# Kernel optimization log

Measured on AMD Instinct MI355X. Metric: run time of the kernel, lower is better.

Reference implementation:

```python
import jax, jax.numpy as jnp
import numpy as np

B, SQ, SKV, D, H = 4, 2048, 2048, 1024, 16
DH = D // H  # 64


def setup_inputs() -> dict:
    key = jax.random.key(0)
    ks = jax.random.split(key, 8)
    s = 0.02  # realistic init scale for weights
    return {
        "query": jax.random.normal(ks[0], (B, SQ, D), dtype=jnp.float32),
        "value": jax.random.normal(ks[1], (B, SKV, D), dtype=jnp.float32),
        "wq": jax.random.normal(ks[2], (H, D, DH), dtype=jnp.float32) * s,
        "bq": jnp.zeros((H, DH), dtype=jnp.float32),
        "wk": jax.random.normal(ks[3], (H, D, DH), dtype=jnp.float32) * s,
        "bk": jnp.zeros((H, DH), dtype=jnp.float32),
        "wv": jax.random.normal(ks[4], (H, D, DH), dtype=jnp.float32) * s,
        "bv": jnp.zeros((H, DH), dtype=jnp.float32),
        "wo": jax.random.normal(ks[5], (D, D), dtype=jnp.float32) * s,
        "bo": jnp.zeros((D,), dtype=jnp.float32),
    }


def reference(query, value, wq, bq, wk, bk, wv, bv, wo, bo):
    # Batched equivalent of the per-head Dense loop: [B,S,D] x [H,D,DH] -> [B,H,S,DH]
    q = jnp.einsum("bsd,hde->bhse", query, wq) + bq[None, :, None, :]
    k = jnp.einsum("bsd,hde->bhse", value, wk) + bk[None, :, None, :]
    v = jnp.einsum("bsd,hde->bhse", value, wv) + bv[None, :, None, :]
    scale = 1.0 / jnp.sqrt(jnp.asarray(DH, dtype=q.dtype))
    scores = jnp.einsum("bhqe,bhke->bhqk", q, k) * scale  # [B,H,SQ,SKV]
    align = jax.nn.softmax(scores, axis=-1)
    heads = jnp.einsum("bhqk,bhke->bhqe", align, v)  # [B,H,SQ,DH]
    # concat heads along feature dim (head order preserved)
    heads = jnp.transpose(heads, (0, 2, 1, 3)).reshape(B, SQ, D)
    return heads @ wo + bo
```

## Files before the change

### kernel.cpp

```cpp
#include <hip/hip_runtime.h>
#include <stdint.h>

#define DEVI __device__ __forceinline__

typedef __bf16  bf16x8 __attribute__((ext_vector_type(8)));
typedef float   f32x4  __attribute__((ext_vector_type(4)));
typedef float   f32x16 __attribute__((ext_vector_type(16)));
typedef uint32_t u32x4 __attribute__((ext_vector_type(4)));
typedef uint32_t u32x2v __attribute__((ext_vector_type(2)));
typedef uint16_t u16x8 __attribute__((ext_vector_type(8)));
typedef uint16_t u16x4 __attribute__((ext_vector_type(4)));

static constexpr int BB = 4, SQL = 2048, SKVL = 2048, DMODEL = 1024, NH = 16;
static constexpr int MROWS = BB * SQL;
static constexpr int KD = DMODEL;

DEVI uint16_t f2bf(float x) {
  uint32_t u = __builtin_bit_cast(uint32_t, x);
  u += 0x7FFFu + ((u >> 16) & 1u);
  return (uint16_t)(u >> 16);
}
DEVI uint32_t cvt2bf(float a, float b) {
  __bf16 x = (__bf16)a, y = (__bf16)b;
  return (uint32_t)__builtin_bit_cast(uint16_t, x) |
         ((uint32_t)__builtin_bit_cast(uint16_t, y) << 16);
}
DEVI f32x4 mfma16(bf16x8 a, bf16x8 b, f32x4 c) {
  return __builtin_amdgcn_mfma_f32_16x16x32_bf16(a, b, c, 0, 0, 0);
}
DEVI f32x16 mfma32(bf16x8 a, bf16x8 b, f32x16 c) {
  return __builtin_amdgcn_mfma_f32_32x32x16_bf16(a, b, c, 0, 0, 0);
}
DEVI void gload16(const void* g, void* l) {
  __builtin_amdgcn_global_load_lds((__attribute__((address_space(1))) const void*)g,
                                   (__attribute__((address_space(3))) void*)l, 16, 0, 0);
}
DEVI bf16x8 ldread(const void* p) { return __builtin_bit_cast(bf16x8, *(const u32x4*)p); }
DEVI u32x2v plswap(uint32_t a, uint32_t b) {
  return __builtin_amdgcn_permlane32_swap(a, b, false, false);
}

__global__ __launch_bounds__(256) void k_cvt(const float* __restrict__ q, const float* __restrict__ v,
                                             const float* __restrict__ wq, const float* __restrict__ wk,
                                             const float* __restrict__ wv, const float* __restrict__ wo,
                                             uint16_t* __restrict__ aq, uint16_t* __restrict__ av,
                                             uint16_t* __restrict__ wt) {
  const int bx = blockIdx.x;
  const int tid = threadIdx.x;
  if (bx < 1024) {
    __shared__ float lds[64 * 65];
    const float* src; int rstride; size_t obase; int d0;
    if (bx < 768) {
      const int zz = bx >> 8, rem = bx & 255, h = rem >> 4, dt = rem & 15;
      d0 = dt * 64;
      src = ((zz == 0) ? wq : (zz == 1) ? wk : wv) + (size_t)h * 65536;
      rstride = 64;
      obase = (size_t)zz * 1048576 + (size_t)h * 64 * 1024;
    } else {
      const int idx = bx - 768, dt = idx >> 4, nt = idx & 15;
      d0 = dt * 64;
      src = wo + nt * 64;
      rstride = 1024;
      obase = (size_t)3 * 1048576 + (size_t)(nt * 64) * 1024;
    }
    const int e4 = (tid & 15) * 4, dl0 = tid >> 4;
    #pragma unroll
    for (int p = 0; p < 4; ++p) {
      const int dl = dl0 + p * 16;
      const float4 x = *(const float4*)(src + (size_t)(d0 + dl) * rstride + e4);
      float* row = &lds[dl * 65 + e4];
      row[0] = x.x; row[1] = x.y; row[2] = x.z; row[3] = x.w;
    }
    __syncthreads();
    const int er = tid >> 2, dp = tid & 3;
    uint16_t tmp[16];
    #pragma unroll
    for (int i = 0; i < 16; ++i) tmp[i] = f2bf(lds[(dp * 16 + i) * 65 + er]);
    uint16_t* orow = wt + obase + (size_t)er * 1024 + d0 + dp * 16;
    u16x8 o0, o1;
    #pragma unroll
    for (int j = 0; j < 8; ++j) { o0[j] = tmp[j]; o1[j] = tmp[8 + j]; }
    *(u16x8*)orow = o0;
    *(u16x8*)(orow + 8) = o1;
  } else {
    const int64_t n4 = (int64_t)MROWS * DMODEL / 4;
    for (int64_t i = (int64_t)(bx - 1024) * 256 + tid; i < 2 * n4; i += (int64_t)2048 * 256) {
      const bool second = (i >= n4);
      const int64_t j = second ? i - n4 : i;
      const float4 x = (second ? (const float4*)v : (const float4*)q)[j];
      u16x4 o = { f2bf(x.x), f2bf(x.y), f2bf(x.z), f2bf(x.w) };
      *(u16x4*)((second ? av : aq) + j * 4) = o;
    }
  }
}

__global__ __launch_bounds__(256) void k_gemm3(const uint16_t* __restrict__ Aq, const uint16_t* __restrict__ Av,
                                               const uint16_t* __restrict__ Wt,
                                               const float* __restrict__ bq, const float* __restrict__ bk,
                                               const float* __restrict__ bv,
                                               uint16_t* __restrict__ Qb, uint16_t* __restrict__ Kb,
                                               uint16_t* __restrict__ Vb, float qscale) {
  __shared__ __align__(16) uint16_t Al[2][128 * 64];
  __shared__ __align__(16) uint16_t Bl[2][128 * 64];
  const int tid = threadIdx.x;
  const int w = tid >> 6, ln = tid & 63;
  const int g = ln >> 4, lc = ln & 15;
  const int seg = blockIdx.y >> 3;
  const int m0 = blockIdx.x * 128, n0 = (blockIdx.y & 7) * 128;
  const uint16_t* A = (seg == 0) ? Aq : Av;
  const uint16_t* Bt = Wt + (size_t)seg * 1048576;
  const float* bias = (seg == 0) ? bq : (seg == 1) ? bk : bv;
  uint16_t* outp = (seg == 0) ? Qb : (seg == 1) ? Kb : Vb;
  const float oscale = (seg == 0) ? qscale : 1.0f;
  const int wm = (w >> 1) * 64, wn = (w & 1) * 64;
  const int srow = w * 32 + (ln >> 3);
  const int colp = (ln & 7) * 16;

  f32x4 acc[4][4] = {};

  auto stage = [&](int kt, int bs) {
    #pragma unroll
    for (int i = 0; i < 4; ++i) {
      const int row = srow + i * 8;
      const int colb = colp ^ ((row & 7) << 4);
      gload16((const char*)(A + (size_t)(m0 + row) * KD + kt * 64) + colb,
              (char*)&Al[bs][0] + w * 4096 + i * 1024);
      gload16((const char*)(Bt + (size_t)(n0 + row) * KD + kt * 64) + colb,
              (char*)&Bl[bs][0] + w * 4096 + i * 1024);
    }
  };

  stage(0, 0);
  asm volatile("s_waitcnt vmcnt(0)" ::: "memory");
  __builtin_amdgcn_s_barrier();
  __builtin_amdgcn_sched_barrier(0);

  int cur = 0;
  #pragma unroll 2
  for (int kt = 0; kt < KD / 64; ++kt) {
    if (kt + 1 < KD / 64) stage(kt + 1, cur ^ 1);
    const char* Ac = (const char*)&Al[cur][0];
    const char* Bc = (const char*)&Bl[cur][0];
    #pragma unroll
    for (int kk = 0; kk < 2; ++kk) {
      bf16x8 af[4], bfr[4];
      #pragma unroll
      for (int mt = 0; mt < 4; ++mt) {
        const int row = wm + mt * 16 + lc;
        af[mt] = ldread(Ac + row * 128 + ((kk * 64 + g * 16) ^ ((row & 7) << 4)));
      }
      #pragma unroll
      for (int nt = 0; nt < 4; ++nt) {
        const int row = wn + nt * 16 + lc;
        bfr[nt] = ldread(Bc + row * 128 + ((kk * 64 + g * 16) ^ ((row & 7) << 4)));
      }
      #pragma unroll
      for (int mt = 0; mt < 4; ++mt)
        #pragma unroll
        for (int nt = 0; nt < 4; ++nt)
          acc[mt][nt] = mfma16(af[mt], bfr[nt], acc[mt][nt]);
    }
    asm volatile("s_waitcnt vmcnt(0)" ::: "memory");
    __builtin_amdgcn_s_barrier();
    __builtin_amdgcn_sched_barrier(0);
    cur ^= 1;
  }

  #pragma unroll
  for (int nt = 0; nt < 4; ++nt) {
    const int n = n0 + wn + nt * 16 + lc;
    const float bv_ = bias[n];
    #pragma unroll
    for (int mt = 0; mt < 4; ++mt) {
      #pragma unroll
      for (int r = 0; r < 4; ++r) {
        const int m = m0 + wm + mt * 16 + g * 4 + r;
        const float val = (acc[mt][nt][r] + bv_) * oscale;
        const int b = m >> 11, s = m & 2047, h = n >> 6, e = n & 63;
        outp[((size_t)((b * NH + h) * SQL + s)) * 64 + e] = f2bf(val);
      }
    }
  }
}

__global__ __launch_bounds__(256) void k_gemmO(const uint16_t* __restrict__ A, const uint16_t* __restrict__ Bt,
                                               const float* __restrict__ bias, float* __restrict__ outp) {
  __shared__ __align__(16) uint16_t Al[2][128 * 64];
  __shared__ __align__(16) uint16_t Bl[2][128 * 64];
  const int tid = threadIdx.x;
  const int w = tid >> 6, ln = tid & 63;
  const int g = ln >> 4, lc = ln & 15;
  const int m0 = blockIdx.x * 128, n0 = blockIdx.y * 128;
  const int wm = (w >> 1) * 64, wn = (w & 1) * 64;
  const int srow = w * 32 + (ln >> 3);
  const int colp = (ln & 7) * 16;

  f32x4 acc[4][4] = {};

  auto stage = [&](int kt, int bs) {
    #pragma unroll
    for (int i = 0; i < 4; ++i) {
      const int row = srow + i * 8;
      const int colb = colp ^ ((row & 7) << 4);
      gload16((const char*)(A + (size_t)(m0 + row) * KD + kt * 64) + colb,
              (char*)&Al[bs][0] + w * 4096 + i * 1024);
      gload16((const char*)(Bt + (size_t)(n0 + row) * KD + kt * 64) + colb,
              (char*)&Bl[bs][0] + w * 4096 + i * 1024);
    }
  };

  stage(0, 0);
  asm volatile("s_waitcnt vmcnt(0)" ::: "memory");
  __builtin_amdgcn_s_barrier();
  __builtin_amdgcn_sched_barrier(0);

  int cur = 0;
  #pragma unroll 2
  for (int kt = 0; kt < KD / 64; ++kt) {
    if (kt + 1 < KD / 64) stage(kt + 1, cur ^ 1);
    const char* Ac = (const char*)&Al[cur][0];
    const char* Bc = (const char*)&Bl[cur][0];
    #pragma unroll
    for (int kk = 0; kk < 2; ++kk) {
      bf16x8 af[4], bfr[4];
      #pragma unroll
      for (int mt = 0; mt < 4; ++mt) {
        const int row = wm + mt * 16 + lc;
        af[mt] = ldread(Ac + row * 128 + ((kk * 64 + g * 16) ^ ((row & 7) << 4)));
      }
      #pragma unroll
      for (int nt = 0; nt < 4; ++nt) {
        const int row = wn + nt * 16 + lc;
        bfr[nt] = ldread(Bc + row * 128 + ((kk * 64 + g * 16) ^ ((row & 7) << 4)));
      }
      #pragma unroll
      for (int mt = 0; mt < 4; ++mt)
        #pragma unroll
        for (int nt = 0; nt < 4; ++nt)
          acc[mt][nt] = mfma16(af[mt], bfr[nt], acc[mt][nt]);
    }
    asm volatile("s_waitcnt vmcnt(0)" ::: "memory");
    __builtin_amdgcn_s_barrier();
    __builtin_amdgcn_sched_barrier(0);
    cur ^= 1;
  }

  #pragma unroll
  for (int nt = 0; nt < 4; ++nt) {
    const int n = n0 + wn + nt * 16 + lc;
    const float bv_ = bias[n];
    #pragma unroll
    for (int mt = 0; mt < 4; ++mt) {
      #pragma unroll
      for (int r = 0; r < 4; ++r) {
        const int m = m0 + wm + mt * 16 + g * 4 + r;
        outp[(size_t)m * DMODEL + n] = acc[mt][nt][r] + bv_;
      }
    }
  }
}

__global__ __launch_bounds__(256, 3) void k_attn(const uint16_t* __restrict__ Qb,
                                                 const uint16_t* __restrict__ Kb,
                                                 const uint16_t* __restrict__ Vb,
                                                 uint16_t* __restrict__ Hd) {
  __shared__ __align__(16) uint16_t Kl[2][64 * 64];
  __shared__ __align__(16) uint16_t Vl[2][64 * 64];
  const int tid = threadIdx.x;
  const int w = tid >> 6, ln = tid & 63;
  const int ql = ln & 31, hi = ln >> 5;
  const int bsw = blockIdx.x;
  const int l = (bsw & 7) * 128 + (bsw >> 3);
  const int qx = l & 15, bh = l >> 4;
  const int q0 = qx * 128 + w * 32;

  const uint16_t* Qp = Qb + ((size_t)bh * SQL + q0 + ql) * 64;
  bf16x8 qf[4];
  #pragma unroll
  for (int s = 0; s < 4; ++s)
    qf[s] = __builtin_bit_cast(bf16x8, *(const u16x8*)(Qp + s * 16 + hi * 8));

  const uint16_t* Kbase = Kb + (size_t)bh * SKVL * 64;
  const uint16_t* Vbase = Vb + (size_t)bh * SKVL * 64;

  const int swl = (ln & 7) << 4;
  const int e0off = (hi << 4) ^ swl;
  const int rb = ql * 128;

  const int krow0 = w * 16 + (ln >> 3);
  const int kcolb = (((ln & 7) ^ (ln >> 3)) << 4);
  const int vkv = (tid & 31) * 2, ve0 = (tid >> 5) * 8;

  f32x16 acc0 = {}, acc1 = {};
  float lsum = 0.f;

  {
    #pragma unroll
    for (int i = 0; i < 2; ++i) {
      const int row = krow0 + i * 8;
      gload16((const char*)(Kbase + (size_t)row * 64) + kcolb,
              (char*)&Kl[0][0] + w * 2048 + i * 1024);
    }
    const u16x8 a = *(const u16x8*)(Vbase + (size_t)vkv * 64 + ve0);
    const u16x8 b = *(const u16x8*)(Vbase + (size_t)(vkv + 1) * 64 + ve0);
    #pragma unroll
    for (int i = 0; i < 8; ++i) {
      const int e = ve0 + i;
      *(uint32_t*)((char*)&Vl[0][0] + e * 128 + ((vkv * 2) ^ ((e & 7) << 4))) =
          (uint32_t)a[i] | ((uint32_t)b[i] << 16);
    }
  }
  __syncthreads();

  int cur = 0;
  for (int t = 0; t < SKVL / 64; ++t) {
    const bool pre = (t + 1 < SKVL / 64);
    u16x8 nv0, nv1;
    if (pre) {
      const uint16_t* Kc = Kbase + (size_t)(t + 1) * 4096;
      #pragma unroll
      for (int i = 0; i < 2; ++i) {
        const int row = krow0 + i * 8;
        gload16((const char*)(Kc + (size_t)row * 64) + kcolb,
                (char*)&Kl[cur ^ 1][0] + w * 2048 + i * 1024);
      }
      const uint16_t* Vc = Vbase + (size_t)(t + 1) * 4096;
      nv0 = *(const u16x8*)(Vc + (size_t)vkv * 64 + ve0);
      nv1 = *(const u16x8*)(Vc + (size_t)(vkv + 1) * 64 + ve0);
    }
    const char* Kc0 = (const char*)&Kl[cur][0];
    f32x16 s0 = {}, s1 = {};
    __builtin_amdgcn_s_setprio(1);
    #pragma unroll
    for (int s = 0; s < 4; ++s) {
      const int off = e0off ^ (s << 5);
      const bf16x8 k0 = ldread(Kc0 + rb + off);
      const bf16x8 k1 = ldread(Kc0 + 4096 + rb + off);
      s0 = mfma32(k0, qf[s], s0);
      s1 = mfma32(k1, qf[s], s1);
    }
    __builtin_amdgcn_s_setprio(0);
    float ps = 0.f;
    #pragma unroll
    for (int r = 0; r < 16; ++r) {
      s0[r] = __builtin_amdgcn_exp2f(s0[r]);
      s1[r] = __builtin_amdgcn_exp2f(s1[r]);
      ps += s0[r] + s1[r];
    }
    lsum += ps;
    uint32_t w32[2][4][2];
    #pragma unroll
    for (int c8 = 0; c8 < 4; ++c8) {
      #pragma unroll
      for (int p = 0; p < 2; ++p) {
        w32[0][c8][p] = cvt2bf(s0[4 * c8 + 2 * p], s0[4 * c8 + 2 * p + 1]);
        w32[1][c8][p] = cvt2bf(s1[4 * c8 + 2 * p], s1[4 * c8 + 2 * p + 1]);
      }
    }
    const char* Vc0 = (const char*)&Vl[cur][0];
    __builtin_amdgcn_s_setprio(1);
    #pragma unroll
    for (int u = 0; u < 4; ++u) {
      const int tt = u >> 1, ul = u & 1;
      const u32x2v e0 = plswap(w32[tt][2 * ul][0], w32[tt][2 * ul + 1][0]);
      const u32x2v e1 = plswap(w32[tt][2 * ul][1], w32[tt][2 * ul + 1][1]);
      u32x4 pj;
      pj[0] = e0[0]; pj[1] = e1[0]; pj[2] = e0[1]; pj[3] = e1[1];
      const bf16x8 pb = __builtin_bit_cast(bf16x8, pj);
      const int off = e0off ^ (u << 5);
      const bf16x8 v0 = ldread(Vc0 + rb + off);
      const bf16x8 v1 = ldread(Vc0 + 4096 + rb + off);
      acc0 = mfma32(v0, pb, acc0);
      acc1 = mfma32(v1, pb, acc1);
    }
    __builtin_amdgcn_s_setprio(0);
    if (pre) {
      #pragma unroll
      for (int i = 0; i < 8; ++i) {
        const int e = ve0 + i;
        *(uint32_t*)((char*)&Vl[cur ^ 1][0] + e * 128 + ((vkv * 2) ^ ((e & 7) << 4))) =
            (uint32_t)nv0[i] | ((uint32_t)nv1[i] << 16);
      }
    }
    __syncthreads();
    cur ^= 1;
  }
  {
    const float lt = lsum + __shfl_xor(lsum, 32);
    const float inv = __builtin_amdgcn_rcpf(lt);
    const int b = bh >> 4, h = bh & 15;
    uint16_t* op = Hd + ((size_t)(b * SQL + q0 + ql)) * DMODEL + h * 64;
    #pragma unroll
    for (int et = 0; et < 2; ++et) {
      #pragma unroll
      for (int r2 = 0; r2 < 8; ++r2) {
        const float v0 = (et ? acc1[2 * r2] : acc0[2 * r2]) * inv;
        const float v1 = (et ? acc1[2 * r2 + 1] : acc0[2 * r2 + 1]) * inv;
        const int e = et * 32 + 4 * hi + (r2 & 1) * 2 + (r2 >> 1) * 8;
        *(uint32_t*)(op + e) = cvt2bf(v0, v1);
      }
    }
  }
}

extern "C" void kernel_launch(void* const* d_in, const int* in_sizes, int n_in,
                              void* d_out, int out_size, void* d_ws, size_t ws_size,
                              hipStream_t stream) {
  const float* query = (const float*)d_in[0];
  const float* value = (const float*)d_in[1];
  const float* wq = (const float*)d_in[2];
  const float* bq = (const float*)d_in[3];
  const float* wk = (const float*)d_in[4];
  const float* bk = (const float*)d_in[5];
  const float* wv = (const float*)d_in[6];
  const float* bv = (const float*)d_in[7];
  const float* wo = (const float*)d_in[8];
  const float* bo = (const float*)d_in[9];

  const size_t SZ_ACT = (size_t)MROWS * DMODEL * 2;
  const size_t SZ_W   = (size_t)4 * DMODEL * DMODEL * 2;
  if (ws_size < 6 * SZ_ACT + SZ_W) return;

  char* ws = (char*)d_ws;
  uint16_t* Aq = (uint16_t*)ws;  ws += SZ_ACT;
  uint16_t* Av = (uint16_t*)ws;  ws += SZ_ACT;
  uint16_t* Wt = (uint16_t*)ws;  ws += SZ_W;
  uint16_t* Qb = (uint16_t*)ws;  ws += SZ_ACT;
  uint16_t* Kb = (uint16_t*)ws;  ws += SZ_ACT;
  uint16_t* Vb = (uint16_t*)ws;  ws += SZ_ACT;
  uint16_t* Hd = (uint16_t*)ws;  ws += SZ_ACT;

  const float QSCALE = 0.18033688011112042f;

  k_cvt<<<dim3(3072), dim3(256), 0, stream>>>(query, value, wq, wk, wv, wo, Aq, Av, Wt);
  k_gemm3<<<dim3(64, 24), dim3(256), 0, stream>>>(Aq, Av, Wt, bq, bk, bv, Qb, Kb, Vb, QSCALE);
  k_attn<<<dim3(1024), dim3(256), 0, stream>>>(Qb, Kb, Vb, Hd);
  k_gemmO<<<dim3(64, 8), dim3(256), 0, stream>>>(Hd, Wt + 3145728, bo, (float*)d_out);
}
```

Baseline: 216.7 us.

## Triple-buffer K tiles with prefetch distance two and refine LDS swizzle

The attention loop's K staging moves from double to triple buffering. Async global-to-LDS loads for K are now issued two tiles ahead, while V stays double-buffered through registers. The generic __syncthreads is replaced by an explicit lgkmcnt wait plus s_barrier, and that barrier is skipped on the last iteration. The XOR swizzle for K and V in LDS is changed, including an extra flip for the second 32-row half, to reduce bank conflicts. Costs and risks: more LDS per block, and ordering only on lgkmcnt may not guarantee the async K loads have landed.

```diff
diff --git a/kernel.cpp b/kernel.cpp
--- a/kernel.cpp
+++ b/kernel.cpp
@@ -264,7 +264,7 @@
                                                  const uint16_t* __restrict__ Kb,
                                                  const uint16_t* __restrict__ Vb,
                                                  uint16_t* __restrict__ Hd) {
-  __shared__ __align__(16) uint16_t Kl[2][64 * 64];
+  __shared__ __align__(16) uint16_t Kl[3][64 * 64];
   __shared__ __align__(16) uint16_t Vl[2][64 * 64];
   const int tid = threadIdx.x;
   const int w = tid >> 6, ln = tid & 63;
@@ -283,59 +283,64 @@
   const uint16_t* Kbase = Kb + (size_t)bh * SKVL * 64;
   const uint16_t* Vbase = Vb + (size_t)bh * SKVL * 64;
 
-  const int swl = (ln & 7) << 4;
+  const int swl = (((ln & 7) ^ ((ln >> 3) & 3)) << 4);
   const int e0off = (hi << 4) ^ swl;
   const int rb = ql * 128;
 
   const int krow0 = w * 16 + (ln >> 3);
-  const int kcolb = (((ln & 7) ^ (ln >> 3)) << 4);
   const int vkv = (tid & 31) * 2, ve0 = (tid >> 5) * 8;
 
   f32x16 acc0 = {}, acc1 = {};
   float lsum = 0.f;
 
+  auto stageK = [&](int t, int buf) {
+    const uint16_t* Kc = Kbase + (size_t)t * 4096;
+    #pragma unroll
+    for (int i = 0; i < 2; ++i) {
+      const int colb = (((ln & 7) ^ (ln >> 3) ^ (w * 2 + i)) << 4);
+      gload16((const char*)(Kc + (size_t)(krow0 + i * 8) * 64) + colb,
+              (char*)&Kl[buf][0] + w * 2048 + i * 1024);
+    }
+  };
+  auto writeV = [&](const u16x8& a, const u16x8& b, int buf) {
+    #pragma unroll
+    for (int i = 0; i < 8; ++i) {
+      const int e = ve0 + i;
+      const int sz = ((i & 7) ^ (tid >> 5)) << 4;
+      *(uint32_t*)((char*)&Vl[buf][0] + e * 128 + ((vkv * 2) ^ sz)) =
+          (uint32_t)a[i] | ((uint32_t)b[i] << 16);
+    }
+  };
+
+  stageK(0, 0);
   {
-    #pragma unroll
-    for (int i = 0; i < 2; ++i) {
-      const int row = krow0 + i * 8;
-      gload16((const char*)(Kbase + (size_t)row * 64) + kcolb,
-              (char*)&Kl[0][0] + w * 2048 + i * 1024);
-    }
     const u16x8 a = *(const u16x8*)(Vbase + (size_t)vkv * 64 + ve0);
     const u16x8 b = *(const u16x8*)(Vbase + (size_t)(vkv + 1) * 64 + ve0);
-    #pragma unroll
-    for (int i = 0; i < 8; ++i) {
-      const int e = ve0 + i;
-      *(uint32_t*)((char*)&Vl[0][0] + e * 128 + ((vkv * 2) ^ ((e & 7) << 4))) =
-          (uint32_t)a[i] | ((uint32_t)b[i] << 16);
-    }
-  }
-  __syncthreads();
-
-  int cur = 0;
+    stageK(1, 1);
+    writeV(a, b, 0);
+  }
+  asm volatile("s_waitcnt lgkmcnt(0)" ::: "memory");
+  __builtin_amdgcn_s_barrier();
+  __builtin_amdgcn_sched_barrier(0);
+
+  int kc = 0, vc = 0;
   for (int t = 0; t < SKVL / 64; ++t) {
     const bool pre = (t + 1 < SKVL / 64);
     u16x8 nv0, nv1;
     if (pre) {
-      const uint16_t* Kc = Kbase + (size_t)(t + 1) * 4096;
-      #pragma unroll
-      for (int i = 0; i < 2; ++i) {
-        const int row = krow0 + i * 8;
-        gload16((const char*)(Kc + (size_t)row * 64) + kcolb,
-                (char*)&Kl[cur ^ 1][0] + w * 2048 + i * 1024);
-      }
       const uint16_t* Vc = Vbase + (size_t)(t + 1) * 4096;
       nv0 = *(const u16x8*)(Vc + (size_t)vkv * 64 + ve0);
       nv1 = *(const u16x8*)(Vc + (size_t)(vkv + 1) * 64 + ve0);
     }
-    const char* Kc0 = (const char*)&Kl[cur][0];
+    if (t + 2 < SKVL / 64) stageK(t + 2, (kc == 0) ? 2 : kc - 1);
+    const char* Kc0 = (const char*)&Kl[kc][0];
     f32x16 s0 = {}, s1 = {};
     __builtin_amdgcn_s_setprio(1);
     #pragma unroll
     for (int s = 0; s < 4; ++s) {
       const int off = e0off ^ (s << 5);
       const bf16x8 k0 = ldread(Kc0 + rb + off);
-      const bf16x8 k1 = ldread(Kc0 + 4096 + rb + off);
+      const bf16x8 k1 = ldread(Kc0 + 4096 + rb + (off ^ 64));
       s0 = mfma32(k0, qf[s], s0);
       s1 = mfma32(k1, qf[s], s1);
     }
@@ -357,7 +362,7 @@
         w32[1][c8][p] = cvt2bf(s1[4 * c8 + 2 * p], s1[4 * c8 + 2 * p + 1]);
       }
     }
-    const char* Vc0 = (const char*)&Vl[cur][0];
+    const char* Vc0 = (const char*)&Vl[vc][0];
     __builtin_amdgcn_s_setprio(1);
     #pragma unroll
     for (int u = 0; u < 4; ++u) {
@@ -369,21 +374,19 @@
       const bf16x8 pb = __builtin_bit_cast(bf16x8, pj);
       const int off = e0off ^ (u << 5);
       const bf16x8 v0 = ldread(Vc0 + rb + off);
-      const bf16x8 v1 = ldread(Vc0 + 4096 + rb + off);
+      const bf16x8 v1 = ldread(Vc0 + 4096 + rb + (off ^ 64));
       acc0 = mfma32(v0, pb, acc0);
       acc1 = mfma32(v1, pb, acc1);
     }
     __builtin_amdgcn_s_setprio(0);
     if (pre) {
-      #pragma unroll
-      for (int i = 0; i < 8; ++i) {
-        const int e = ve0 + i;
-        *(uint32_t*)((char*)&Vl[cur ^ 1][0] + e * 128 + ((vkv * 2) ^ ((e & 7) << 4))) =
-            (uint32_t)nv0[i] | ((uint32_t)nv1[i] << 16);
-      }
-    }
-    __syncthreads();
-    cur ^= 1;
+      writeV(nv0, nv1, vc ^ 1);
+      asm volatile("s_waitcnt lgkmcnt(0)" ::: "memory");
+      __builtin_amdgcn_s_barrier();
+      __builtin_amdgcn_sched_barrier(0);
+    }
+    kc = (kc == 2) ? 0 : kc + 1;
+    vc ^= 1;
   }
   {
     const float lt = lsum + __shfl_xor(lsum, 32);
```

Result: slower. 223.5 us (+3.1%).
